# Performance work log

Measured on AMD Instinct MI355X. Metric: run time of the kernel, lower is better.

## Reference

```python
import jax, jax.numpy as jnp
import numpy as np

B, L, D, H = 4, 2048, 1024, 16
DH = D // H  # 64
MASK_VALUE = -1000000.0
EPS = 1e-12


def setup_inputs() -> dict:
    key = jax.random.key(0)
    ks = jax.random.split(key, 7)
    s = 1.0 / np.sqrt(D)
    x = jax.random.normal(ks[0], (B, L, D), dtype=jnp.float32)
    Wq = jax.random.uniform(ks[1], (D, H * DH), jnp.float32, -s, s)
    Wk = jax.random.uniform(ks[2], (D, H * DH), jnp.float32, -s, s)
    Wv = jax.random.uniform(ks[3], (D, H * DH), jnp.float32, -s, s)
    Wo = jax.random.uniform(ks[4], (H * DH, D), jnp.float32, -s, s)
    gamma = jnp.ones((D,), jnp.float32)
    beta = jnp.zeros((D,), jnp.float32)
    # causal mask: True positions are masked (query m cannot attend to key n > m)
    attn_mask = jnp.triu(jnp.ones((L, L), dtype=bool), k=1)
    return {"x": x, "Wq": Wq, "Wk": Wk, "Wv": Wv, "Wo": Wo,
            "gamma": gamma, "beta": beta, "attn_mask": attn_mask}


def _layernorm(y, gamma, beta):
    mu = jnp.mean(y, axis=-1, keepdims=True)
    var = jnp.mean(jnp.square(y - mu), axis=-1, keepdims=True)
    return (y - mu) * jax.lax.rsqrt(var + EPS) * gamma + beta


def reference(x, Wq, Wk, Wv, Wo, gamma, beta, attn_mask):
    scale = 1.0 / np.sqrt(DH)
    # projections, reshape to heads: B L (H D) -> B H L D
    q = (x @ Wq).reshape(B, L, H, DH).transpose(0, 2, 1, 3)
    k = (x @ Wk).reshape(B, L, H, DH).transpose(0, 2, 1, 3)
    v = (x @ Wv).reshape(B, L, H, DH).transpose(0, 2, 1, 3)
    scores = jnp.einsum('bhmd,bhnd->bhmn', q, k) * scale
    scores = jnp.where(attn_mask, MASK_VALUE, scores)
    probs = jax.nn.softmax(scores, axis=-1)
    z = jnp.einsum('bhmn,bhnd->bhmd', probs, v)
    z = z.transpose(0, 2, 1, 3).reshape(B, L, H * DH)
    out = jax.nn.relu(z @ Wo)
    return _layernorm(out + x, gamma, beta)
```

## Files before the change

### kernel.cpp

```cpp
#include <hip/hip_runtime.h>
#include <math.h>

#define B_ 4
#define L_ 2048
#define D_ 1024
#define H_ 16
#define DH_ 64
#define QKV_N 3072

typedef unsigned short ushort_t;
typedef unsigned int uint_t;
using bf16x8 = __attribute__((ext_vector_type(8))) short;
using f32x4  = __attribute__((ext_vector_type(4))) float;

__device__ __forceinline__ ushort_t f2bf(float f) {
    union { float f; unsigned int u; } v; v.f = f;
    unsigned int u = v.u;
    unsigned int rnd = ((u >> 16) & 1u) + 0x7fffu;
    return (ushort_t)((u + rnd) >> 16);
}

__device__ __forceinline__ float bf2f(ushort_t u) {
    union { unsigned int u; float f; } v;
    v.u = ((unsigned int)u) << 16;
    return v.f;
}

__device__ __forceinline__ void glds16(const void* g, void* l) {
    __builtin_amdgcn_global_load_lds(
        (const __attribute__((address_space(1))) unsigned int*)g,
        (__attribute__((address_space(3))) unsigned int*)l, 16, 0, 0);
}

__global__ __launch_bounds__(256) void prep(const float* __restrict__ Wq,
                                            const float* __restrict__ Wk,
                                            const float* __restrict__ Wv,
                                            const float* __restrict__ Wo,
                                            const float* __restrict__ x,
                                            ushort_t* __restrict__ wcat,
                                            ushort_t* __restrict__ wto,
                                            ushort_t* __restrict__ xb) {
    const int t = threadIdx.x;
    if (blockIdx.z == 4) {
        const int bid = blockIdx.y * 16 + blockIdx.x;
        const int base = bid * 32768 + t * 4;
        #pragma unroll
        for (int it = 0; it < 32; ++it) {
            float4 v = *(const float4*)(x + base + it * 1024);
            ushort4 o;
            o.x = f2bf(v.x); o.y = f2bf(v.y); o.z = f2bf(v.z); o.w = f2bf(v.w);
            *(ushort4*)(xb + base + it * 1024) = o;
        }
        return;
    }
    __shared__ ushort_t tile[64][65];
    const int widx = blockIdx.z;
    const float* W = (widx == 0) ? Wq : (widx == 1) ? Wk : (widx == 2) ? Wv : Wo;
    ushort_t* dst = (widx < 3) ? (wcat + (size_t)widx * 1024 * 1024) : wto;
    const int j = t & 63, i0 = t >> 6;
    const int kbase = blockIdx.y * 64, nbase = blockIdx.x * 64;
    #pragma unroll
    for (int it = 0; it < 16; ++it) {
        int i = it * 4 + i0;
        tile[i][j] = f2bf(W[(size_t)(kbase + i) * 1024 + nbase + j]);
    }
    __syncthreads();
    #pragma unroll
    for (int it = 0; it < 16; ++it) {
        int nn = it * 4 + i0;
        dst[(size_t)(nbase + nn) * 1024 + kbase + j] = tile[j][nn];
    }
}

__global__ __launch_bounds__(512) void gemm8p(const ushort_t* __restrict__ A,
                                              const ushort_t* __restrict__ Wt,
                                              ushort_t* __restrict__ Cbf,
                                              const ushort_t* __restrict__ resid,
                                              ushort_t* __restrict__ vt,
                                              int M, int N, int K, int fuse) {
    __shared__ ushort_t lds[49152];
    const int t = threadIdx.x;
    const int w = t >> 6, ln = t & 63;
    const int l15 = ln & 15, quad = ln >> 4;
    const int wrow = w >> 1, wcol = w & 1;

    int bx = blockIdx.x, by = blockIdx.y;
    {
        int nwg = gridDim.x * gridDim.y;
        if ((nwg & 7) == 0) {
            int flat = by * gridDim.x + bx;
            int nid = (flat & 7) * (nwg >> 3) + (flat >> 3);
            by = nid / gridDim.x;
            bx = nid - by * gridDim.x;
        }
    }
    const int bm = by * 256, bn = bx * 128;

    const ushort_t* Agp[2];
    const ushort_t* Bgp;
    #pragma unroll
    for (int j = 0; j < 2; ++j) {
        int r = j * 128 + (t >> 2);
        int c = (t & 3) ^ ((r >> 1) & 3);
        Agp[j] = A + (size_t)(bm + r) * K + c * 8;
    }
    {
        int r = t >> 2;
        int c = (t & 3) ^ ((r >> 1) & 3);
        Bgp = Wt + (size_t)(bn + r) * K + c * 8;
    }

    const int swz8 = (quad ^ ((l15 >> 1) & 3)) * 8;
    int aoff[4], boff[4];
    #pragma unroll
    for (int mf = 0; mf < 4; ++mf)
        aoff[mf] = (wrow * 64 + mf * 16 + l15) * 32 + swz8;
    #pragma unroll
    for (int nf = 0; nf < 4; ++nf)
        boff[nf] = (wcol * 64 + nf * 16 + l15) * 32 + swz8;

    f32x4 acc[4][4] = {};
    const int NT = K >> 6;

#define ABASE(BUF, KH) ((BUF) * 24576 + (KH) * 12288)
#define BBASE(BUF, KH) (ABASE(BUF, KH) + 8192)

#define STAGE(BUF, KH, KT) do {                                             \
        glds16(Agp[0] + (KT) * 64 + (KH) * 32, &lds[ABASE(BUF, KH) + t * 8]);\
        glds16(Agp[1] + (KT) * 64 + (KH) * 32,                              \
               &lds[ABASE(BUF, KH) + 4096 + t * 8]);                        \
        glds16(Bgp + (KT) * 64 + (KH) * 32, &lds[BBASE(BUF, KH) + t * 8]);  \
    } while (0)

#define VM6 asm volatile("s_waitcnt vmcnt(6)" ::: "memory")
#define VM3 asm volatile("s_waitcnt vmcnt(3)" ::: "memory")
#define VM0 asm volatile("s_waitcnt vmcnt(0)" ::: "memory")
#define NOVM ((void)0)

#define PHASE(BUF, KH, STAGEC, VMW) do {                                    \
        bf16x8 af_[4], bf_[4];                                              \
        _Pragma("unroll")                                                   \
        for (int m_ = 0; m_ < 4; ++m_)                                      \
            af_[m_] = *(const bf16x8*)&lds[ABASE(BUF, KH) + aoff[m_]];      \
        _Pragma("unroll")                                                   \
        for (int n_ = 0; n_ < 4; ++n_)                                      \
            bf_[n_] = *(const bf16x8*)&lds[BBASE(BUF, KH) + boff[n_]];      \
        STAGEC;                                                             \
        VMW;                                                                \
        __builtin_amdgcn_s_barrier();                                       \
        asm volatile("s_waitcnt lgkmcnt(0)" ::: "memory");                  \
        __builtin_amdgcn_s_setprio(1);                                      \
        _Pragma("unroll")                                                   \
        for (int m_ = 0; m_ < 4; ++m_)                                      \
            _Pragma("unroll")                                               \
            for (int n_ = 0; n_ < 4; ++n_)                                  \
                acc[m_][n_] = __builtin_amdgcn_mfma_f32_16x16x32_bf16(      \
                    af_[m_], bf_[n_], acc[m_][n_], 0, 0, 0);                \
        __builtin_amdgcn_s_setprio(0);                                      \
        __builtin_amdgcn_s_barrier();                                       \
    } while (0)

    STAGE(0, 0, 0);
    STAGE(0, 1, 0);
    STAGE(1, 0, 1);
    VM6;
    __builtin_amdgcn_s_barrier();

    for (int it = 0; it < (NT >> 1) - 1; ++it) {
        const int kt1 = 2 * it + 1, kt2 = 2 * it + 2, kt3 = 2 * it + 3;
        PHASE(0, 0, STAGE(1, 1, kt1), VM6);
        PHASE(0, 1, STAGE(0, 0, kt2), VM6);
        PHASE(1, 0, STAGE(0, 1, kt2), VM6);
        PHASE(1, 1, STAGE(1, 0, kt3), VM6);
    }

    PHASE(0, 0, STAGE(1, 1, NT - 1), VM6);
    PHASE(0, 1, NOVM, VM3);
    PHASE(1, 0, NOVM, VM0);
    PHASE(1, 1, NOVM, NOVM);

#undef PHASE
#undef STAGE
#undef ABASE
#undef BBASE

    if (vt && bn >= 2048) {
        #pragma unroll
        for (int mf = 0; mf < 4; ++mf) {
            #pragma unroll
            for (int nf = 0; nf < 4; ++nf) {
                #pragma unroll
                for (int reg = 0; reg < 4; ++reg) {
                    int row = bm + wrow * 64 + mf * 16 + quad * 4 + reg;
                    int col = bn + wcol * 64 + nf * 16 + l15 - 2048;
                    int bb = row >> 11, tok = row & 2047;
                    int h = col >> 6, d = col & 63;
                    int tg = tok & 63;
                    int sc = (tg & 15) * 4 + (tg >> 4);
                    size_t addr = ((size_t)((bb * 16 + h) * 64 + d) << 11)
                                + (tok & ~63) + sc;
                    vt[addr] = f2bf(acc[mf][nf][reg]);
                }
            }
        }
    } else {
        #pragma unroll
        for (int mf = 0; mf < 4; ++mf) {
            #pragma unroll
            for (int nf = 0; nf < 4; ++nf) {
                #pragma unroll
                for (int reg = 0; reg < 4; ++reg) {
                    int row = bm + wrow * 64 + mf * 16 + quad * 4 + reg;
                    int col = bn + wcol * 64 + nf * 16 + l15;
                    size_t idx = (size_t)row * N + col;
                    float v = acc[mf][nf][reg];
                    if (fuse) v = fmaxf(v, 0.f) + bf2f(resid[idx]);
                    Cbf[idx] = f2bf(v);
                }
            }
        }
    }
}

__global__ __launch_bounds__(256) void gemm_mfma(const ushort_t* __restrict__ A,
                                                 const ushort_t* __restrict__ Wt,
                                                 ushort_t* __restrict__ Cbf,
                                                 const ushort_t* __restrict__ resid,
                                                 ushort_t* __restrict__ vt,
                                                 int M, int N, int K, int fuse) {
    __shared__ ushort_t As[128 * 64];
    __shared__ ushort_t Bs[128 * 64];
    const int t = threadIdx.x;
    const int w = t >> 6, ln = t & 63;
    const int l15 = ln & 15, quad = ln >> 4;
    const int bm = blockIdx.y * 128, bn = blockIdx.x * 128;
    const int wm = (w & 1) * 64, wn = (w >> 1) * 64;

    const ushort_t* Ap[4];
    const ushort_t* Bp[4];
    #pragma unroll
    for (int j = 0; j < 4; ++j) {
        const int i = t + j * 256;
        const int r = i >> 3;
        const int qg = (i & 7) ^ (r & 7);
        Ap[j] = A  + (size_t)(bm + r) * K + qg * 8;
        Bp[j] = Wt + (size_t)(bn + r) * K + qg * 8;
    }

    f32x4 acc[4][4] = {};

    for (int k0 = 0; k0 < K; k0 += 64) {
        __syncthreads();
        #pragma unroll
        for (int j = 0; j < 4; ++j) {
            glds16(Ap[j] + k0, &As[(t + j * 256) * 8]);
            glds16(Bp[j] + k0, &Bs[(t + j * 256) * 8]);
        }
        __syncthreads();

        #pragma unroll
        for (int kw = 0; kw < 2; ++kw) {
            bf16x8 af[4], bfr[4];
            #pragma unroll
            for (int im = 0; im < 4; ++im) {
                int row = wm + im * 16 + l15;
                int phys = (kw * 4 + quad) ^ (row & 7);
                af[im] = *(const bf16x8*)&As[row * 64 + phys * 8];
            }
            #pragma unroll
            for (int in = 0; in < 4; ++in) {
                int row = wn + in * 16 + l15;
                int phys = (kw * 4 + quad) ^ (row & 7);
                bfr[in] = *(const bf16x8*)&Bs[row * 64 + phys * 8];
            }
            #pragma unroll
            for (int im = 0; im < 4; ++im)
                #pragma unroll
                for (int in = 0; in < 4; ++in)
                    acc[im][in] = __builtin_amdgcn_mfma_f32_16x16x32_bf16(
                        af[im], bfr[in], acc[im][in], 0, 0, 0);
        }
    }

    if (vt && bn >= 2048) {
        #pragma unroll
        for (int im = 0; im < 4; ++im) {
            #pragma unroll
            for (int in = 0; in < 4; ++in) {
                #pragma unroll
                for (int reg = 0; reg < 4; ++reg) {
                    int row = bm + wm + im * 16 + quad * 4 + reg;
                    int col = bn + wn + in * 16 + l15 - 2048;
                    int bb = row >> 11, tok = row & 2047;
                    int h = col >> 6, d = col & 63;
                    int tg = tok & 63;
                    int sc = (tg & 15) * 4 + (tg >> 4);
                    size_t addr = ((size_t)((bb * 16 + h) * 64 + d) << 11)
                                + (tok & ~63) + sc;
                    vt[addr] = f2bf(acc[im][in][reg]);
                }
            }
        }
    } else {
        #pragma unroll
        for (int im = 0; im < 4; ++im) {
            #pragma unroll
            for (int in = 0; in < 4; ++in) {
                #pragma unroll
                for (int reg = 0; reg < 4; ++reg) {
                    int row = bm + wm + im * 16 + quad * 4 + reg;
                    int col = bn + wn + in * 16 + l15;
                    size_t idx = (size_t)row * N + col;
                    float v = acc[im][in][reg];
                    if (fuse) v = fmaxf(v, 0.f) + bf2f(resid[idx]);
                    Cbf[idx] = f2bf(v);
                }
            }
        }
    }
}

__global__ __launch_bounds__(256) void attn_mfma(const ushort_t* __restrict__ qkv,
                                                 const ushort_t* __restrict__ Vt,
                                                 ushort_t* __restrict__ Zb) {
    __shared__ ushort_t Ks[128 * 64];
    __shared__ ushort_t Vs[64 * 128];
    __shared__ ushort_t Ps[4][32 * 72];
    const int t = threadIdx.x, w = t >> 6, ln = t & 63;
    const int l15 = ln & 15, quad = ln >> 4;
    const int bh = blockIdx.x;
    const int b = bh >> 4, h = bh & 15;
    const int Qt = 15 - blockIdx.y;

    bf16x8 ones;
    #pragma unroll
    for (int i = 0; i < 8; ++i) ones[i] = (short)0x3f80;

    int kkey[4], kq[4], vd[4], vcq[4];
    #pragma unroll
    for (int j = 0; j < 4; ++j) {
        int i = t + j * 256;
        kkey[j] = i >> 3;
        kq[j]   = (i & 7) ^ (kkey[j] & 7);
        vd[j]   = i >> 4;
        int cqp = i & 15;
        vcq[j]  = (cqp & 8) | ((cqp & 7) ^ (vd[j] & 7));
    }
    const ushort_t* Kgb = qkv + 1024 + (size_t)b * L_ * QKV_N + h * DH_;
    const ushort_t* Vgb = Vt + (size_t)((b * H_ + h) * DH_) * L_;

    bf16x8 qf[2][2];
    #pragma unroll
    for (int mt = 0; mt < 2; ++mt) {
        const ushort_t* qrow =
            qkv + (size_t)(b * L_ + Qt * 128 + w * 32 + mt * 16 + l15) * QKV_N + h * DH_;
        qf[mt][0] = *(const bf16x8*)(qrow + quad * 8);
        qf[mt][1] = *(const bf16x8*)(qrow + 32 + quad * 8);
    }

    f32x4 acc_o[2][4] = {};
    f32x4 l_acc[2] = {};

    const float c2 = 0.18033688f;

    for (int kt = 0; kt <= Qt; ++kt) {
        __syncthreads();
        #pragma unroll
        for (int j = 0; j < 4; ++j) {
            glds16(Kgb + (size_t)(kt * 128 + kkey[j]) * QKV_N + kq[j] * 8,
                   &Ks[(t + j * 256) * 8]);
            glds16(Vgb + (size_t)vd[j] * L_ + kt * 128 + vcq[j] * 8,
                   &Vs[(t + j * 256) * 8]);
        }
        __syncthreads();

        const bool masked = (kt == Qt);

        #pragma unroll
        for (int ph = 0; ph < 2; ++ph) {
            if (masked && ph && w < 2) continue;

            f32x4 acc_s[2][4] = {};
            __builtin_amdgcn_s_setprio(1);
            #pragma unroll
            for (int in = 0; in < 4; ++in) {
                const int key = ph * 64 + in * 16 + l15;
                #pragma unroll
                for (int ks = 0; ks < 2; ++ks) {
                    int phys = (ks * 4 + quad) ^ (key & 7);
                    bf16x8 kf = *(const bf16x8*)&Ks[key * 64 + phys * 8];
                    acc_s[0][in] = __builtin_amdgcn_mfma_f32_16x16x32_bf16(
                        qf[0][ks], kf, acc_s[0][in], 0, 0, 0);
                    acc_s[1][in] = __builtin_amdgcn_mfma_f32_16x16x32_bf16(
                        qf[1][ks], kf, acc_s[1][in], 0, 0, 0);
                }
            }
            __builtin_amdgcn_s_setprio(0);

            #pragma unroll
            for (int mt = 0; mt < 2; ++mt) {
                #pragma unroll
                for (int reg = 0; reg < 4; ++reg) {
                    const int row = mt * 16 + quad * 4 + reg;
                    float pv[4];
                    #pragma unroll
                    for (int in = 0; in < 4; ++in) {
                        float s2 = fmaf(acc_s[mt][in][reg], c2, -2.0f);
                        if (masked) {
                            int col = kt * 128 + ph * 64 + in * 16 + l15;
                            int qg  = Qt * 128 + w * 32 + row;
                            s2 = (col > qg) ? -100000.0f : s2;
                        }
                        pv[in] = __builtin_amdgcn_exp2f(s2);
                    }
                    uint_t u01 = __builtin_amdgcn_perm(
                        __float_as_uint(pv[1]), __float_as_uint(pv[0]), 0x07060302u);
                    uint_t u23 = __builtin_amdgcn_perm(
                        __float_as_uint(pv[3]), __float_as_uint(pv[2]), 0x07060302u);
                    uint2* dst = (uint2*)&Ps[w][row * 72 + l15 * 4];
                    *dst = make_uint2(u01, u23);
                }
            }

            __builtin_amdgcn_s_setprio(1);
            #pragma unroll
            for (int ks = 0; ks < 2; ++ks) {
                bf16x8 pf0 = *(const bf16x8*)&Ps[w][(l15) * 72 + ks * 32 + quad * 8];
                bf16x8 pf1 = *(const bf16x8*)&Ps[w][(16 + l15) * 72 + ks * 32 + quad * 8];
                #pragma unroll
                for (int in = 0; in < 4; ++in) {
                    const int d = in * 16 + l15;
                    int physv = ph * 8 + (((ks * 4 + quad) ^ (d & 7)));
                    bf16x8 vf = *(const bf16x8*)&Vs[d * 128 + physv * 8];
                    acc_o[0][in] = __builtin_amdgcn_mfma_f32_16x16x32_bf16(
                        vf, pf0, acc_o[0][in], 0, 0, 0);
                    acc_o[1][in] = __builtin_amdgcn_mfma_f32_16x16x32_bf16(
                        vf, pf1, acc_o[1][in], 0, 0, 0);
                }
                l_acc[0] = __builtin_amdgcn_mfma_f32_16x16x32_bf16(ones, pf0, l_acc[0], 0, 0, 0);
                l_acc[1] = __builtin_amdgcn_mfma_f32_16x16x32_bf16(ones, pf1, l_acc[1], 0, 0, 0);
            }
            __builtin_amdgcn_s_setprio(0);
        }
    }

    #pragma unroll
    for (int mt = 0; mt < 2; ++mt) {
        const float inv = 1.0f / l_acc[mt][0];
        const int row = b * L_ + Qt * 128 + w * 32 + mt * 16 + l15;
        #pragma unroll
        for (int in = 0; in < 4; ++in) {
            const int dbase = h * DH_ + in * 16 + quad * 4;
            f32x4 a = acc_o[mt][in];
            ushort4 o;
            o.x = f2bf(a[0] * inv); o.y = f2bf(a[1] * inv);
            o.z = f2bf(a[2] * inv); o.w = f2bf(a[3] * inv);
            *(ushort4*)(Zb + (size_t)row * D_ + dbase) = o;
        }
    }
}

__global__ __launch_bounds__(64) void ln_kernel(const ushort_t* __restrict__ Y,
                                                const float* __restrict__ gamma,
                                                const float* __restrict__ beta,
                                                float* __restrict__ out) {
    const int row = blockIdx.x;
    const int t = threadIdx.x;
    const ushort_t* y = Y + (size_t)row * D_;

    float v[16];
    #pragma unroll
    for (int s = 0; s < 4; ++s) {
        ushort4 u = *(const ushort4*)(y + s * 256 + t * 4);
        v[s * 4 + 0] = bf2f(u.x);
        v[s * 4 + 1] = bf2f(u.y);
        v[s * 4 + 2] = bf2f(u.z);
        v[s * 4 + 3] = bf2f(u.w);
    }

    float sum = 0.f;
    #pragma unroll
    for (int i = 0; i < 16; ++i) sum += v[i];
    #pragma unroll
    for (int k = 1; k < 64; k <<= 1) sum += __shfl_xor(sum, k, 64);
    const float mu = sum * (1.f / (float)D_);

    float var = 0.f;
    #pragma unroll
    for (int i = 0; i < 16; ++i) {
        float d = v[i] - mu;
        var += d * d;
    }
    #pragma unroll
    for (int k = 1; k < 64; k <<= 1) var += __shfl_xor(var, k, 64);
    const float rstd = rsqrtf(var * (1.f / (float)D_) + 1e-12f);

    #pragma unroll
    for (int s = 0; s < 4; ++s) {
        const int col = s * 256 + t * 4;
        float4 g  = *(const float4*)(gamma + col);
        float4 bb = *(const float4*)(beta + col);
        float4 o;
        o.x = (v[s * 4 + 0] - mu) * rstd * g.x + bb.x;
        o.y = (v[s * 4 + 1] - mu) * rstd * g.y + bb.y;
        o.z = (v[s * 4 + 2] - mu) * rstd * g.z + bb.z;
        o.w = (v[s * 4 + 3] - mu) * rstd * g.w + bb.w;
        *(float4*)(out + (size_t)row * D_ + col) = o;
    }
}

extern "C" void kernel_launch(void* const* d_in, const int* in_sizes, int n_in,
                              void* d_out, int out_size, void* d_ws, size_t ws_size,
                              hipStream_t stream) {
    const float* x     = (const float*)d_in[0];
    const float* Wq    = (const float*)d_in[1];
    const float* Wk    = (const float*)d_in[2];
    const float* Wv    = (const float*)d_in[3];
    const float* Wo    = (const float*)d_in[4];
    const float* gamma = (const float*)d_in[5];
    const float* beta  = (const float*)d_in[6];
    float* out = (float*)d_out;

    char* ws = (char*)d_ws;
    ushort_t* x_bf = (ushort_t*)(ws);
    ushort_t* wcat = (ushort_t*)(ws + (16u  << 20));
    ushort_t* wto  = (ushort_t*)(ws + (22u  << 20));
    ushort_t* qkv  = (ushort_t*)(ws + (24u  << 20));
    ushort_t* vt   = (ushort_t*)(ws + (72u  << 20));
    ushort_t* z_bf = (ushort_t*)(ws + (88u  << 20));
    ushort_t* y_bf = (ushort_t*)(ws + (104u << 20));

    const int M = B_ * L_;

    prep<<<dim3(16, 16, 5), 256, 0, stream>>>(Wq, Wk, Wv, Wo, x, wcat, wto, x_bf);

    gemm8p<<<dim3(QKV_N / 128, M / 256), 512, 0, stream>>>(
        x_bf, wcat, qkv, nullptr, vt, M, QKV_N, D_, 0);

    attn_mfma<<<dim3(B_ * H_, 16), 256, 0, stream>>>(qkv, vt, z_bf);

    gemm_mfma<<<dim3(D_ / 128, M / 128), 256, 0, stream>>>(
        z_bf, wto, y_bf, x_bf, nullptr, M, D_, D_, 1);

    ln_kernel<<<M, 64, 0, stream>>>(y_bf, gamma, beta, out);
}
```

Before: 275.9 us.

## Replace half-tile ping-pong in QKV GEMM with three-buffer full-tile ring

The QKV projection GEMM now keeps a three-slot LDS ring of full 64-wide K tiles instead of a two-buffer scheme of half tiles. Each phase reads both K halves and issues 32 MFMAs, while loads for two tiles ahead are in flight. This halves the number of barrier pairs per K step and lengthens the prefetch distance. The cost is LDS use rising from 96KB to 144KB per workgroup and more live fragment registers, which may reduce occupancy.

```diff
diff --git a/kernel.cpp b/kernel.cpp
--- a/kernel.cpp
+++ b/kernel.cpp
@@ -72,13 +72,13 @@
     }
 }
 
-__global__ __launch_bounds__(512) void gemm8p(const ushort_t* __restrict__ A,
-                                              const ushort_t* __restrict__ Wt,
-                                              ushort_t* __restrict__ Cbf,
-                                              const ushort_t* __restrict__ resid,
-                                              ushort_t* __restrict__ vt,
-                                              int M, int N, int K, int fuse) {
-    __shared__ ushort_t lds[49152];
+__global__ __launch_bounds__(512) void gemm_ring3(const ushort_t* __restrict__ A,
+                                                  const ushort_t* __restrict__ Wt,
+                                                  ushort_t* __restrict__ Cbf,
+                                                  const ushort_t* __restrict__ resid,
+                                                  ushort_t* __restrict__ vt,
+                                                  int M, int N, int K, int fuse) {
+    __shared__ ushort_t lds[73728];
     const int t = threadIdx.x;
     const int w = t >> 6, ln = t & 63;
     const int l15 = ln & 15, quad = ln >> 4;
@@ -122,67 +122,64 @@
     f32x4 acc[4][4] = {};
     const int NT = K >> 6;
 
-#define ABASE(BUF, KH) ((BUF) * 24576 + (KH) * 12288)
-#define BBASE(BUF, KH) (ABASE(BUF, KH) + 8192)
-
-#define STAGE(BUF, KH, KT) do {                                             \
-        glds16(Agp[0] + (KT) * 64 + (KH) * 32, &lds[ABASE(BUF, KH) + t * 8]);\
-        glds16(Agp[1] + (KT) * 64 + (KH) * 32,                              \
-               &lds[ABASE(BUF, KH) + 4096 + t * 8]);                        \
-        glds16(Bgp + (KT) * 64 + (KH) * 32, &lds[BBASE(BUF, KH) + t * 8]);  \
+#define STAGE6(BASE, KT) do {                                               \
+        glds16(Agp[0] + (KT) * 64,      &lds[(BASE) + t * 8]);              \
+        glds16(Agp[1] + (KT) * 64,      &lds[(BASE) + 4096 + t * 8]);       \
+        glds16(Agp[0] + (KT) * 64 + 32, &lds[(BASE) + 8192 + t * 8]);       \
+        glds16(Agp[1] + (KT) * 64 + 32, &lds[(BASE) + 12288 + t * 8]);      \
+        glds16(Bgp + (KT) * 64,         &lds[(BASE) + 16384 + t * 8]);      \
+        glds16(Bgp + (KT) * 64 + 32,    &lds[(BASE) + 20480 + t * 8]);      \
     } while (0)
 
 #define VM6 asm volatile("s_waitcnt vmcnt(6)" ::: "memory")
-#define VM3 asm volatile("s_waitcnt vmcnt(3)" ::: "memory")
 #define VM0 asm volatile("s_waitcnt vmcnt(0)" ::: "memory")
 #define NOVM ((void)0)
 
-#define PHASE(BUF, KH, STAGEC, VMW) do {                                    \
-        bf16x8 af_[4], bf_[4];                                              \
+#define PHASE(CUR, STAGEC, VMW, ENDBAR) do {                                \
+        bf16x8 af_[2][4], bf_[2][4];                                        \
         _Pragma("unroll")                                                   \
-        for (int m_ = 0; m_ < 4; ++m_)                                      \
-            af_[m_] = *(const bf16x8*)&lds[ABASE(BUF, KH) + aoff[m_]];      \
-        _Pragma("unroll")                                                   \
-        for (int n_ = 0; n_ < 4; ++n_)                                      \
-            bf_[n_] = *(const bf16x8*)&lds[BBASE(BUF, KH) + boff[n_]];      \
+        for (int kh_ = 0; kh_ < 2; ++kh_) {                                 \
+            _Pragma("unroll")                                               \
+            for (int m_ = 0; m_ < 4; ++m_)                                  \
+                af_[kh_][m_] = *(const bf16x8*)                             \
+                    &lds[(CUR) + kh_ * 8192 + aoff[m_]];                    \
+            _Pragma("unroll")                                               \
+            for (int n_ = 0; n_ < 4; ++n_)                                  \
+                bf_[kh_][n_] = *(const bf16x8*)                             \
+                    &lds[(CUR) + 16384 + kh_ * 4096 + boff[n_]];            \
+        }                                                                   \
         STAGEC;                                                             \
         VMW;                                                                \
         __builtin_amdgcn_s_barrier();                                       \
         asm volatile("s_waitcnt lgkmcnt(0)" ::: "memory");                  \
         __builtin_amdgcn_s_setprio(1);                                      \
         _Pragma("unroll")                                                   \
-        for (int m_ = 0; m_ < 4; ++m_)                                      \
+        for (int kh_ = 0; kh_ < 2; ++kh_)                                   \
             _Pragma("unroll")                                               \
-            for (int n_ = 0; n_ < 4; ++n_)                                  \
-                acc[m_][n_] = __builtin_amdgcn_mfma_f32_16x16x32_bf16(      \
-                    af_[m_], bf_[n_], acc[m_][n_], 0, 0, 0);                \
+            for (int m_ = 0; m_ < 4; ++m_)                                  \
+                _Pragma("unroll")                                           \
+                for (int n_ = 0; n_ < 4; ++n_)                              \
+                    acc[m_][n_] = __builtin_amdgcn_mfma_f32_16x16x32_bf16(  \
+                        af_[kh_][m_], bf_[kh_][n_], acc[m_][n_], 0, 0, 0);  \
         __builtin_amdgcn_s_setprio(0);                                      \
-        __builtin_amdgcn_s_barrier();                                       \
+        if (ENDBAR) __builtin_amdgcn_s_barrier();                           \
     } while (0)
 
-    STAGE(0, 0, 0);
-    STAGE(0, 1, 0);
-    STAGE(1, 0, 1);
+    STAGE6(0, 0);
+    STAGE6(24576, 1);
     VM6;
     __builtin_amdgcn_s_barrier();
 
-    for (int it = 0; it < (NT >> 1) - 1; ++it) {
-        const int kt1 = 2 * it + 1, kt2 = 2 * it + 2, kt3 = 2 * it + 3;
-        PHASE(0, 0, STAGE(1, 1, kt1), VM6);
-        PHASE(0, 1, STAGE(0, 0, kt2), VM6);
-        PHASE(1, 0, STAGE(0, 1, kt2), VM6);
-        PHASE(1, 1, STAGE(1, 0, kt3), VM6);
-    }
-
-    PHASE(0, 0, STAGE(1, 1, NT - 1), VM6);
-    PHASE(0, 1, NOVM, VM3);
-    PHASE(1, 0, NOVM, VM0);
-    PHASE(1, 1, NOVM, NOVM);
+    int cur = 0, nb1 = 24576, nb2 = 49152;
+    for (int T = 0; T < NT - 2; ++T) {
+        PHASE(cur, STAGE6(nb2, T + 2), VM6, 1);
+        int tmp = cur; cur = nb1; nb1 = nb2; nb2 = tmp;
+    }
+    PHASE(cur, NOVM, VM0, 1);
+    PHASE(nb1, NOVM, NOVM, 0);
 
 #undef PHASE
-#undef STAGE
-#undef ABASE
-#undef BBASE
+#undef STAGE6
 
     if (vt && bn >= 2048) {
         #pragma unroll
@@ -534,7 +531,7 @@
 
     prep<<<dim3(16, 16, 5), 256, 0, stream>>>(Wq, Wk, Wv, Wo, x, wcat, wto, x_bf);
 
-    gemm8p<<<dim3(QKV_N / 128, M / 256), 512, 0, stream>>>(
+    gemm_ring3<<<dim3(QKV_N / 128, M / 256), 512, 0, stream>>>(
         x_bf, wcat, qkv, nullptr, vt, M, QKV_N, D_, 0);
 
     attn_mfma<<<dim3(B_ * H_, 16), 256, 0, stream>>>(qkv, vt, z_bf);
```

New measurement: 278.6 us. Within noise of the previous version (+1.0%).
